# Kernel optimization log

Hardware: AMD Instinct MI355X
Metric: run time of the kernel (lower is better)

The kernel has to match this reference:

```python
import jax, jax.numpy as jnp
import numpy as np


def setup_inputs() -> dict:
    key = jax.random.key(0)
    B, C, T, F = 16, 2, 1000, 257
    k1, = jax.random.split(key, 1)
    inp = jax.random.normal(k1, (B, C, T, F, 2), dtype=jnp.float32)
    weights = jnp.ones((1, C, 1, F, 1), dtype=jnp.float32)   # init constant 1
    bias = jnp.zeros((1, C, 1, F, 1), dtype=jnp.float32)     # init constant 0
    alpha = jnp.full((1, C, F, 1), -4.0, dtype=jnp.float32)  # init constant -4
    s_1 = jnp.zeros((B, C, F, 1), dtype=jnp.float32)
    return {"input": inp, "weights": weights, "bias": bias, "alpha": alpha, "s_1": s_1}


def reference(input, weights, bias, alpha, s_1):
    # input: [B, C, T, F, 2]
    in_data2 = jnp.sum(input ** 2, axis=-1, keepdims=True)  # [B, C, T, F, 1]
    a = jax.nn.sigmoid(alpha)                               # [1, C, F, 1]

    def step(s, x):
        s = s * (1.0 - a) + x * a   # EMA over time, per (c, f)
        return s, s

    # scan over time axis -> move T to leading axis
    xs = jnp.moveaxis(in_data2, 2, 0)          # [T, B, C, F, 1]
    s_last, smooth = jax.lax.scan(step, s_1, xs)
    smooth = jnp.sqrt(jnp.moveaxis(smooth, 0, 2))  # [B, C, T, F, 1]

    res = input / (smooth + 1e-8) * weights + bias
    return res, s_last
```

## Files before the change

kernel.cpp:

```cpp
#include <hip/hip_runtime.h>

#define BB 16
#define CC 2
#define TT 1000
#define FF 257
#define NCHAIN (BB * CC * FF)
#define RES_ELEMS ((size_t)BB * CC * TT * FF * 2)

#define CPB 8
#define KCH 64
#define LCH 16

__global__ __launch_bounds__(512, 8) void fnorm_kernel(
    const float* __restrict__ input,
    const float* __restrict__ weights,
    const float* __restrict__ bias,
    const float* __restrict__ alpha,
    const float* __restrict__ s1,
    float* __restrict__ out)
{
    const int tx = threadIdx.x;
    const int k  = threadIdx.y;
    const int chain = blockIdx.x * CPB + tx;

    const int f  = chain % FF;
    const int bc = chain / FF;
    const int c  = bc % CC;
    const int cf = c * FF + f;

    const float2* __restrict__ in2 = (const float2*)input + (size_t)bc * (TT * FF) + f;
    float2* __restrict__ out2      = (float2*)out        + (size_t)bc * (TT * FF) + f;

    const float av = 1.0f / (1.0f + __expf(-alpha[cf]));
    const float om = 1.0f - av;
    const float w  = weights[cf];
    const float bi = bias[cf];

    const int t0  = k * LCH;
    const int rem = TT - t0;
    const int n   = rem < LCH ? (rem < 0 ? 0 : rem) : LCH;

    float2 x[LCH];
    #pragma unroll
    for (int t = 0; t < LCH; ++t)
        if (t < n) x[t] = in2[(size_t)(t0 + t) * FF];

    float s = 0.0f;
    float p = 1.0f;
    #pragma unroll
    for (int t = 0; t < LCH; ++t) {
        if (t < n) {
            float2 v = x[t];
            float d2 = fmaf(v.x, v.x, v.y * v.y);
            s = fmaf(d2, av, s * om);
            p *= om;
        }
    }

    __shared__ float p_s[KCH][CPB + 1];
    __shared__ float e_s[KCH][CPB + 1];
    __shared__ float i_s[KCH][CPB + 1];
    p_s[k][tx] = p;
    e_s[k][tx] = s;
    __syncthreads();
    {
        const int tid = k * CPB + tx;
        const int wv  = tid >> 6;
        const int ln  = tid & 63;
        float pp = p_s[ln][wv];
        float ee = e_s[ln][wv];
        #pragma unroll
        for (int d = 1; d < 64; d <<= 1) {
            float pu = __shfl_up(pp, d, 64);
            float eu = __shfl_up(ee, d, 64);
            if (ln >= d) { ee = fmaf(pp, eu, ee); pp *= pu; }
        }
        const float S0 = s1[blockIdx.x * CPB + wv];
        float Sin = fmaf(pp, S0, ee);
        float Sex = __shfl_up(Sin, 1, 64);
        if (ln == 0) Sex = S0;
        i_s[ln][wv] = Sex;
        if (ln == 63) out[RES_ELEMS + (size_t)(blockIdx.x * CPB + wv)] = Sin;
    }
    __syncthreads();

    s = i_s[k][tx];
    #pragma unroll
    for (int t = 0; t < LCH; ++t) {
        if (t < n) {
            float2 v = x[t];
            float d2 = fmaf(v.x, v.x, v.y * v.y);
            s = fmaf(d2, av, s * om);
            float inv = __frsqrt_rn(s + 1e-16f) * w;
            float2 y;
            y.x = fmaf(v.x, inv, bi);
            y.y = fmaf(v.y, inv, bi);
            out2[(size_t)(t0 + t) * FF] = y;
        }
    }
}

extern "C" void kernel_launch(void* const* d_in, const int* in_sizes, int n_in,
                              void* d_out, int out_size, void* d_ws, size_t ws_size,
                              hipStream_t stream) {
    const float* input   = (const float*)d_in[0];
    const float* weights = (const float*)d_in[1];
    const float* bias    = (const float*)d_in[2];
    const float* alpha   = (const float*)d_in[3];
    const float* s1      = (const float*)d_in[4];
    float* out = (float*)d_out;

    dim3 block(CPB, KCH);
    dim3 grid(NCHAIN / CPB);
    hipLaunchKernelGGL(fnorm_kernel, grid, block, 0, stream,
                       input, weights, bias, alpha, s1, out);
}
```

Before: 155.5 us.

## Process frequency pairs with float4 accesses and split odd bin into separate kernel

After: 158.5 us. No clear change (+1.9%).

```diff
diff --git a/kernel.cpp b/kernel.cpp
--- a/kernel.cpp
+++ b/kernel.cpp
@@ -4,14 +4,17 @@
 #define CC 2
 #define TT 1000
 #define FF 257
-#define NCHAIN (BB * CC * FF)
+#define NBC (BB * CC)
+#define NCHAIN (NBC * FF)
 #define RES_ELEMS ((size_t)BB * CC * TT * FF * 2)
 
-#define CPB 8
+#define FPB 8
 #define KCH 64
 #define LCH 16
+#define NPAIR (NBC * 128)
+#define NBLK (NPAIR / FPB)
 
-__global__ __launch_bounds__(512, 8) void fnorm_kernel(
+__global__ __launch_bounds__(512, 4) void fnorm_main(
     const float* __restrict__ input,
     const float* __restrict__ weights,
     const float* __restrict__ bias,
@@ -20,77 +23,147 @@
     float* __restrict__ out)
 {
     const int tx = threadIdx.x;
-    const int k  = threadIdx.y;
-    const int chain = blockIdx.x * CPB + tx;
+    const int ky = threadIdx.y;
+    const int P  = blockIdx.x * FPB + tx;
+    const int bc = P >> 7;
+    const int f  = (P & 127) * 2;
+    const int cf = (bc & 1) * FF + f;
 
-    const int f  = chain % FF;
-    const int bc = chain / FF;
-    const int c  = bc % CC;
-    const int cf = c * FF + f;
+    const float av_a = 1.0f / (1.0f + __expf(-alpha[cf]));
+    const float av_b = 1.0f / (1.0f + __expf(-alpha[cf + 1]));
+    const float om_a = 1.0f - av_a, om_b = 1.0f - av_b;
+    const float w_a = weights[cf],  w_b = weights[cf + 1];
+    const float bi_a = bias[cf],    bi_b = bias[cf + 1];
 
-    const float2* __restrict__ in2 = (const float2*)input + (size_t)bc * (TT * FF) + f;
-    float2* __restrict__ out2      = (float2*)out        + (size_t)bc * (TT * FF) + f;
+    const float* __restrict__ ibase = input + (size_t)bc * (TT * FF * 2) + 2 * f;
+    float* __restrict__ obase       = out   + (size_t)bc * (TT * FF * 2) + 2 * f;
+
+    const int t0 = ky * LCH;
+    const int n  = (TT - t0) < LCH ? ((TT - t0) < 0 ? 0 : (TT - t0)) : LCH;
+
+    float4 x[LCH];
+    #pragma unroll
+    for (int t = 0; t < LCH; ++t)
+        if (t < n) x[t] = *(const float4*)(ibase + (size_t)(t0 + t) * (FF * 2));
+
+    float sa = 0.f, sb = 0.f, pa = 1.f, pb = 1.f;
+    #pragma unroll
+    for (int t = 0; t < LCH; ++t) {
+        if (t < n) {
+            float4 v = x[t];
+            sa = fmaf(fmaf(v.x, v.x, v.y * v.y), av_a, sa * om_a); pa *= om_a;
+            sb = fmaf(fmaf(v.z, v.z, v.w * v.w), av_b, sb * om_b); pb *= om_b;
+        }
+    }
+
+    __shared__ float p_s[KCH][2 * FPB + 1];
+    __shared__ float e_s[KCH][2 * FPB + 1];
+    __shared__ float i_s[KCH][2 * FPB + 1];
+    p_s[ky][2 * tx] = pa;  p_s[ky][2 * tx + 1] = pb;
+    e_s[ky][2 * tx] = sa;  e_s[ky][2 * tx + 1] = sb;
+    __syncthreads();
+    {
+        const int tid  = tx + ky * FPB;
+        const int lane = tid & 63;
+        const int wv   = tid >> 6;
+        #pragma unroll
+        for (int h = 0; h < 2; ++h) {
+            const int ch = wv + 8 * h;
+            const int Pc = blockIdx.x * FPB + (ch >> 1);
+            const int chain = (Pc >> 7) * FF + (Pc & 127) * 2 + (ch & 1);
+            float pp = p_s[lane][ch];
+            float ee = e_s[lane][ch];
+            #pragma unroll
+            for (int d = 1; d < 64; d <<= 1) {
+                float pu = __shfl_up(pp, d, 64);
+                float eu = __shfl_up(ee, d, 64);
+                if (lane >= d) { ee = fmaf(pp, eu, ee); pp *= pu; }
+            }
+            const float S0 = s1[chain];
+            float Sin = fmaf(pp, S0, ee);
+            float Sex = __shfl_up(Sin, 1, 64);
+            if (lane == 0) Sex = S0;
+            i_s[lane][ch] = Sex;
+            if (lane == 63) out[RES_ELEMS + (size_t)chain] = Sin;
+        }
+    }
+    __syncthreads();
+
+    float s_a = i_s[ky][2 * tx], s_b = i_s[ky][2 * tx + 1];
+    #pragma unroll
+    for (int t = 0; t < LCH; ++t) {
+        if (t < n) {
+            float4 v = x[t];
+            s_a = fmaf(fmaf(v.x, v.x, v.y * v.y), av_a, s_a * om_a);
+            s_b = fmaf(fmaf(v.z, v.z, v.w * v.w), av_b, s_b * om_b);
+            float ia = __frsqrt_rn(s_a + 1e-16f) * w_a;
+            float ib = __frsqrt_rn(s_b + 1e-16f) * w_b;
+            float4 y;
+            y.x = fmaf(v.x, ia, bi_a); y.y = fmaf(v.y, ia, bi_a);
+            y.z = fmaf(v.z, ib, bi_b); y.w = fmaf(v.w, ib, bi_b);
+            *(float4*)(obase + (size_t)(t0 + t) * (FF * 2)) = y;
+        }
+    }
+}
+
+__global__ __launch_bounds__(512) void fnorm_straggler(
+    const float* __restrict__ input,
+    const float* __restrict__ weights,
+    const float* __restrict__ bias,
+    const float* __restrict__ alpha,
+    const float* __restrict__ s1,
+    float* __restrict__ out)
+{
+    const int wv   = threadIdx.x >> 6;
+    const int lane = threadIdx.x & 63;
+    const int bc   = blockIdx.x * 8 + wv;
+    const int f    = FF - 1;
+    const int cf   = (bc & 1) * FF + f;
+    const int chain = bc * FF + f;
 
     const float av = 1.0f / (1.0f + __expf(-alpha[cf]));
     const float om = 1.0f - av;
     const float w  = weights[cf];
     const float bi = bias[cf];
 
-    const int t0  = k * LCH;
-    const int rem = TT - t0;
-    const int n   = rem < LCH ? (rem < 0 ? 0 : rem) : LCH;
+    const float2* __restrict__ in2 = (const float2*)input + (size_t)bc * (TT * FF) + f;
+    float2* __restrict__ out2      = (float2*)out        + (size_t)bc * (TT * FF) + f;
 
-    float2 x[LCH];
+    const int t0 = lane * 16;
+    const int n  = (TT - t0) < 16 ? ((TT - t0) < 0 ? 0 : (TT - t0)) : 16;
+
+    float2 x[16];
     #pragma unroll
-    for (int t = 0; t < LCH; ++t)
+    for (int t = 0; t < 16; ++t)
         if (t < n) x[t] = in2[(size_t)(t0 + t) * FF];
 
-    float s = 0.0f;
-    float p = 1.0f;
+    float ee = 0.f, pp = 1.f;
     #pragma unroll
-    for (int t = 0; t < LCH; ++t) {
+    for (int t = 0; t < 16; ++t) {
         if (t < n) {
             float2 v = x[t];
-            float d2 = fmaf(v.x, v.x, v.y * v.y);
-            s = fmaf(d2, av, s * om);
-            p *= om;
+            ee = fmaf(fmaf(v.x, v.x, v.y * v.y), av, ee * om);
+            pp *= om;
         }
     }
+    #pragma unroll
+    for (int d = 1; d < 64; d <<= 1) {
+        float pu = __shfl_up(pp, d, 64);
+        float eu = __shfl_up(ee, d, 64);
+        if (lane >= d) { ee = fmaf(pp, eu, ee); pp *= pu; }
+    }
+    const float S0 = s1[chain];
+    float Sin = fmaf(pp, S0, ee);
+    float Sex = __shfl_up(Sin, 1, 64);
+    if (lane == 0) Sex = S0;
+    if (lane == 63) out[RES_ELEMS + (size_t)chain] = Sin;
 
-    __shared__ float p_s[KCH][CPB + 1];
-    __shared__ float e_s[KCH][CPB + 1];
-    __shared__ float i_s[KCH][CPB + 1];
-    p_s[k][tx] = p;
-    e_s[k][tx] = s;
-    __syncthreads();
-    {
-        const int tid = k * CPB + tx;
-        const int wv  = tid >> 6;
-        const int ln  = tid & 63;
-        float pp = p_s[ln][wv];
-        float ee = e_s[ln][wv];
-        #pragma unroll
-        for (int d = 1; d < 64; d <<= 1) {
-            float pu = __shfl_up(pp, d, 64);
-            float eu = __shfl_up(ee, d, 64);
-            if (ln >= d) { ee = fmaf(pp, eu, ee); pp *= pu; }
-        }
-        const float S0 = s1[blockIdx.x * CPB + wv];
-        float Sin = fmaf(pp, S0, ee);
-        float Sex = __shfl_up(Sin, 1, 64);
-        if (ln == 0) Sex = S0;
-        i_s[ln][wv] = Sex;
-        if (ln == 63) out[RES_ELEMS + (size_t)(blockIdx.x * CPB + wv)] = Sin;
-    }
-    __syncthreads();
-
-    s = i_s[k][tx];
+    float s = Sex;
     #pragma unroll
-    for (int t = 0; t < LCH; ++t) {
+    for (int t = 0; t < 16; ++t) {
         if (t < n) {
             float2 v = x[t];
-            float d2 = fmaf(v.x, v.x, v.y * v.y);
-            s = fmaf(d2, av, s * om);
+            s = fmaf(fmaf(v.x, v.x, v.y * v.y), av, s * om);
             float inv = __frsqrt_rn(s + 1e-16f) * w;
             float2 y;
             y.x = fmaf(v.x, inv, bi);
@@ -110,8 +183,8 @@
     const float* s1      = (const float*)d_in[4];
     float* out = (float*)d_out;
 
-    dim3 block(CPB, KCH);
-    dim3 grid(NCHAIN / CPB);
-    hipLaunchKernelGGL(fnorm_kernel, grid, block, 0, stream,
+    hipLaunchKernelGGL(fnorm_straggler, dim3(4), dim3(512), 0, stream,
+                       input, weights, bias, alpha, s1, out);
+    hipLaunchKernelGGL(fnorm_main, dim3(NBLK), dim3(FPB, KCH), 0, stream,
                        input, weights, bias, alpha, s1, out);
 }
```
